# Optimization experiments

Measured on AMD Instinct MI355X. Metric: run time of the kernel, lower is better.

The kernel has to match this reference:

```python
import jax, jax.numpy as jnp
import numpy as np

NUM_HEADS = 8


def _proj(W, b, x):
    # x: [B, C, N] channel-wise 1x1 conv == matmul over channels
    return jnp.einsum('oc,bcn->bon', W, x) + b[None, :, None]


def setup_inputs() -> dict:
    key = jax.random.key(0)
    ks = jax.random.split(key, 8)
    B, C, H, W = 4, 512, 24, 24
    inp = {
        'feat0': jax.random.normal(ks[0], (B, C, H, W), jnp.float32),
        'feat1': jax.random.normal(ks[1], (B, C, H, W), jnp.float32),
        'feat2': jax.random.normal(ks[2], (B, C, H, W), jnp.float32),
        'Wq': jax.random.normal(ks[3], (C, C), jnp.float32) * 0.02,
        'bq': jnp.zeros((C,), jnp.float32),
        'Wk': jax.random.normal(ks[4], (C, C), jnp.float32) * 0.02,
        'bk': jnp.zeros((C,), jnp.float32),
        'Wv': jax.random.normal(ks[5], (C, C), jnp.float32) * 0.02,
        'bv': jnp.zeros((C,), jnp.float32),
        'Wo': jax.random.normal(ks[6], (C, C), jnp.float32) * 0.02,
        'bo': jnp.zeros((C,), jnp.float32),
    }
    return inp


def reference(feat0, feat1, feat2, Wq, bq, Wk, bk, Wv, bv, Wo, bo):
    feats = [feat0, feat1, feat2]
    B, C, H, W = feat0.shape
    h = NUM_HEADS
    d = C // h
    scale = d ** -0.5

    # Precompute K/V once per feature (the torch loop redundantly recomputes them;
    # the math is identical).
    flat = [f.reshape(B, C, H * W) for f in feats]
    K = jnp.concatenate([_proj(Wk, bk, x).reshape(B, h, d, -1) for x in flat], axis=-1)  # [B,h,d,KV]
    V = jnp.concatenate([_proj(Wv, bv, x).reshape(B, h, d, -1) for x in flat], axis=-1)  # [B,h,d,KV]

    outs = []
    for feat, x in zip(feats, flat):
        q = _proj(Wq, bq, x).reshape(B, h, d, H * W)  # [B,h,d,N]
        attn = jax.nn.softmax(jnp.einsum('bhdn,bhdm->bhnm', q, K) * scale, axis=-1)
        out = jnp.einsum('bhnm,bhdm->bhdn', attn, V).reshape(B, C, H * W)
        out = _proj(Wo, bo, out).reshape(B, C, H, W)
        outs.append(feat + out)
    return tuple(outs)
```

## Files before the change

kernel.cpp:

```cpp
#include <hip/hip_runtime.h>


using bf16x8 = __attribute__((ext_vector_type(8))) short;
using f32x4  = __attribute__((ext_vector_type(4))) float;
using f32x16 = __attribute__((ext_vector_type(16))) float;
using u32x4  = __attribute__((ext_vector_type(4))) unsigned int;
using u16x4  = __attribute__((ext_vector_type(4))) unsigned short;
using u16x8  = __attribute__((ext_vector_type(8))) unsigned short;

#define MFMA16(a, b, c) __builtin_amdgcn_mfma_f32_16x16x32_bf16((a), (b), (c), 0, 0, 0)
#define MFMA32(a, b, c) __builtin_amdgcn_mfma_f32_32x32x16_bf16((a), (b), (c), 0, 0, 0)

__device__ __forceinline__ unsigned short f2bf(float f) {
  unsigned int u = __float_as_uint(f);
  return (unsigned short)((u + 0x7fffu + ((u >> 16) & 1u)) >> 16);
}

__device__ __forceinline__ f32x16 zero16() {
  f32x16 z;
#pragma unroll
  for (int i = 0; i < 16; ++i) z[i] = 0.f;
  return z;
}

__global__ __launch_bounds__(256) void k_prep(
    const float* __restrict__ Wq, const float* __restrict__ Wk,
    const float* __restrict__ Wv, const float* __restrict__ Wo,
    const float* __restrict__ f0, const float* __restrict__ f1,
    const float* __restrict__ f2,
    unsigned short* __restrict__ Wf, unsigned short* __restrict__ Xf) {
  __shared__ unsigned short tile[64][65];
  const int bid = blockIdx.x;
  const int t = threadIdx.x;
  if (bid < 1024) {
    int idx = (bid * 256 + t) * 4;
    int p   = idx >> 18;
    int rem = idx & 262143;
    int o = rem >> 9, c0 = rem & 511;
    const float* s = p == 0 ? Wq : p == 1 ? Wk : p == 2 ? Wv : Wo;
    f32x4 v = *(const f32x4*)(s + rem);
    u16x4 pk;
    pk[0] = f2bf(v[0]); pk[1] = f2bf(v[1]); pk[2] = f2bf(v[2]); pk[3] = f2bf(v[3]);
    int mt = o >> 6, fr = (o & 63) >> 4, lr = o & 15;
    int ks = c0 >> 5, lg = (c0 & 31) >> 3, j0 = c0 & 7;
    size_t off = (size_t)((((p * 8 + mt) * 16 + ks) * 4 + fr)) * 512 +
                 (lg * 16 + lr) * 8 + j0;
    *(u16x4*)(Wf + off) = pk;
    return;
  }
  const int id = bid - 1024;
  const int nt = id % 9;
  const int ct = (id / 9) % 8;
  const int z  = id / 72;
  const int b = z / 3, f = z % 3;
  const float* src = (f == 0 ? f0 : f == 1 ? f1 : f2) + b * (512 * 576);

#pragma unroll
  for (int i = 0; i < 16; ++i) {
    int idx = i * 256 + t;
    int cc = idx >> 6, nn = idx & 63;
    tile[cc][nn] = f2bf(src[(ct * 64 + cc) * 576 + nt * 64 + nn]);
  }
  __syncthreads();
  const int ntw = f * 9 + nt;
#pragma unroll
  for (int i = 0; i < 4; ++i) {
    int slot = i * 256 + t;
    int nn = slot >> 4, cq = slot & 15;
    int cl = cq * 4;
    int c  = ct * 64 + cl;
    int fc = nn >> 4, lr = nn & 15;
    int ks = c >> 5, lg = (c & 31) >> 3, j0 = c & 7;
    u16x4 pk;
    pk[0] = tile[cl][nn]; pk[1] = tile[cl + 1][nn];
    pk[2] = tile[cl + 2][nn]; pk[3] = tile[cl + 3][nn];
    size_t off = (size_t)((((b * 27 + ntw) * 16 + ks) * 4 + fc)) * 512 +
                 (lg * 16 + lr) * 8 + j0;
    *(u16x4*)(Xf + off) = pk;
  }
}

__global__ __launch_bounds__(256) void k_gemm_qkv(
    const unsigned short* __restrict__ Wf, const unsigned short* __restrict__ Xf,
    const float* __restrict__ bq, const float* __restrict__ bk,
    const float* __restrict__ bv,
    unsigned short* __restrict__ Qf, unsigned short* __restrict__ Kf,
    unsigned short* __restrict__ Vf) {
  const int id = blockIdx.x;
  const int xcd = id & 7, s = id >> 3;
  const int b = xcd >> 1, par = xcd & 1;
  const int p = s / 54, bx = (s % 54) * 2 + par;
  const int t = threadIdx.x, w = t >> 6, l = t & 63, lg = l >> 4, lr = l & 15;
  const int wid = bx * 4 + w;
  const int mt = wid / 54, rest = wid % 54;
  const int ntw = rest >> 1, half = rest & 1;
  const unsigned short* A = Wf + (size_t)(p * 8 + mt) * 16 * 2048 + l * 8;
  const unsigned short* B = Xf + (size_t)(b * 27 + ntw) * 16 * 2048 +
                            half * 1024 + l * 8;

  f32x4 acc[4][2];
#pragma unroll
  for (int fr = 0; fr < 4; ++fr)
#pragma unroll
    for (int fc = 0; fc < 2; ++fc) acc[fr][fc] = (f32x4){0.f, 0.f, 0.f, 0.f};

#pragma unroll 2
  for (int ks = 0; ks < 16; ++ks) {
    bf16x8 af[4], bfv[2];
#pragma unroll
    for (int fr = 0; fr < 4; ++fr)
      af[fr] = *(const bf16x8*)(A + ks * 2048 + fr * 512);
#pragma unroll
    for (int fc = 0; fc < 2; ++fc)
      bfv[fc] = *(const bf16x8*)(B + ks * 2048 + fc * 512);
#pragma unroll
    for (int fr = 0; fr < 4; ++fr)
#pragma unroll
      for (int fc = 0; fc < 2; ++fc)
        acc[fr][fc] = MFMA16(af[fr], bfv[fc], acc[fr][fc]);
  }

  const float* bias = p == 0 ? bq : p == 1 ? bk : bv;
  const int bh = b * 8 + mt;
  const int ck = ntw * 2 + half;
#pragma unroll
  for (int fr = 0; fr < 4; ++fr) {
    f32x4 b4 = *(const f32x4*)(bias + mt * 64 + fr * 16 + lg * 4);
#pragma unroll
    for (int fc = 0; fc < 2; ++fc) {
      if (p < 2) {
        unsigned short* outF = (p == 0) ? Qf : Kf;
        u16x4 pk;
#pragma unroll
        for (int r = 0; r < 4; ++r) {
          float v = acc[fr][fc][r] + b4[r];
          if (p == 0) v *= 0.18033688f;
          pk[r] = f2bf(v);
        }
        size_t off = ((size_t)bh * 54 + ck) * 2048 + fr * 512 +
                     ((lg >> 1) * 32 + fc * 16 + lr) * 8 + (lg & 1) * 4;
        *(u16x4*)(outF + off) = pk;
      } else {
        size_t base = ((size_t)bh * 54 + ck) * 2048 +
                      ((fr >> 1) * 2 + fc) * 512 +
                      (((lr >> 3) & 1) * 32 + (fr & 1) * 16 + lg * 4) * 8 +
                      (lr & 7);
#pragma unroll
        for (int r = 0; r < 4; ++r)
          Vf[base + r * 8] = f2bf(acc[fr][fc][r] + b4[r]);
      }
    }
  }
}

__device__ __forceinline__ void softmax_pa(const f32x16& s, float& lsum,
                                           bf16x8& pa0, bf16x8& pa1, int hi) {
  unsigned int W[8];
  float a0 = 0.f, a1 = 0.f;
#pragma unroll
  for (int u = 0; u < 8; ++u) {
    float e0, e1;
    asm("v_exp_f32 %0, %1" : "=v"(e0) : "v"(s[2 * u]));
    asm("v_exp_f32 %0, %1" : "=v"(e1) : "v"(s[2 * u + 1]));
    a0 += e0; a1 += e1;
    asm("v_cvt_pk_bf16_f32 %0, %1, %2" : "=v"(W[u]) : "v"(e0), "v"(e1));
  }
  lsum += a0 + a1;
  unsigned int fw[2][4];
#pragma unroll
  for (int kf = 0; kf < 2; ++kf)
#pragma unroll
    for (int wd = 0; wd < 2; ++wd) {
      unsigned int lo  = W[4 * kf + wd];
      unsigned int hw  = W[4 * kf + 2 + wd];
      unsigned int pub = hi ? lo : hw;
      unsigned int rcv = (unsigned int)__shfl_xor((int)pub, 32, 64);
      fw[kf][wd]     = hi ? rcv : lo;
      fw[kf][2 + wd] = hi ? hw : rcv;
    }
  u32x4 w0, w1;
  w0[0] = fw[0][0]; w0[1] = fw[0][1]; w0[2] = fw[0][2]; w0[3] = fw[0][3];
  w1[0] = fw[1][0]; w1[1] = fw[1][1]; w1[2] = fw[1][2]; w1[3] = fw[1][3];
  pa0 = __builtin_bit_cast(bf16x8, w0);
  pa1 = __builtin_bit_cast(bf16x8, w1);
}

__global__ __launch_bounds__(128, 4) void k_attn(
    const unsigned short* __restrict__ Qf, const unsigned short* __restrict__ Kf,
    const unsigned short* __restrict__ Vf, unsigned short* __restrict__ Of) {
  const int id = blockIdx.x;
  const int xcd = id & 7, slot = id >> 3;
  const int bh = xcd * 4 + (slot / 54);
  const int qt = slot % 54;
  const int b = bh >> 3, h = bh & 7;
  const int t = threadIdx.x, w = t >> 6, l = t & 63;
  const int lr = l & 31, hi = l >> 5;

  __shared__ float Obuf[2][32][68];
  __shared__ float Lbuf[2][32];

  const unsigned short* Qb = Qf + ((size_t)bh * 54 + qt) * 2048 + l * 8;
  bf16x8 bq[4];
#pragma unroll
  for (int kf = 0; kf < 4; ++kf) bq[kf] = *(const bf16x8*)(Qb + kf * 512);

  f32x16 oacc[2];
  oacc[0] = zero16(); oacc[1] = zero16();
  float ls = 0.f;

  const unsigned short* Kb = Kf + (size_t)bh * 54 * 2048 + l * 8;
  const unsigned short* Vb = Vf + (size_t)bh * 54 * 2048 + l * 8;

#pragma unroll 1
  for (int ck = w; ck < 54; ck += 2) {
    const unsigned short* kc = Kb + ck * 2048;
    const unsigned short* vc = Vb + ck * 2048;
    bf16x8 ak[4];
#pragma unroll
    for (int i = 0; i < 4; ++i) ak[i] = *(const bf16x8*)(kc + i * 512);

    f32x16 sA = zero16();
#pragma unroll
    for (int kf = 0; kf < 4; ++kf) sA = MFMA32(ak[kf], bq[kf], sA);

    bf16x8 vb[4];
#pragma unroll
    for (int i = 0; i < 4; ++i) vb[i] = *(const bf16x8*)(vc + i * 512);

    bf16x8 pa0, pa1;
    softmax_pa(sA, ls, pa0, pa1, hi);

    oacc[0] = MFMA32(pa0, vb[0], oacc[0]);
    oacc[0] = MFMA32(pa1, vb[1], oacc[0]);
    oacc[1] = MFMA32(pa0, vb[2], oacc[1]);
    oacc[1] = MFMA32(pa1, vb[3], oacc[1]);
  }

  float lt = ls + __shfl_xor(ls, 32, 64);
  if (l < 32) Lbuf[w][lr] = lt;
#pragma unroll
  for (int dt = 0; dt < 2; ++dt)
#pragma unroll
    for (int r = 0; r < 16; ++r)
      Obuf[w][(r & 3) + 8 * (r >> 2) + 4 * hi][dt * 32 + lr] = oacc[dt][r];
  __syncthreads();

  const int n = t >> 2, dq = t & 3;
  float ltot = Lbuf[0][n] + Lbuf[1][n];
  float linv = 1.0f / ltot;
#pragma unroll
  for (int part = 0; part < 2; ++part) {
    const int d0 = dq * 16 + part * 8;
    u16x8 o8;
#pragma unroll
    for (int i = 0; i < 8; ++i) {
      float ov = Obuf[0][n][d0 + i] + Obuf[1][n][d0 + i];
      o8[i] = f2bf(ov * linv);
    }
    size_t off = (size_t)((((b * 27 + (qt >> 1)) * 16 + h * 2 + (d0 >> 5)) * 4 +
                           (qt & 1) * 2 + (n >> 4))) * 512 +
                 ((d0 >> 3) & 3) * 128 + (n & 15) * 8;
    *(u16x8*)(Of + off) = o8;
  }
}

__global__ __launch_bounds__(256) void k_gemm_out(
    const unsigned short* __restrict__ Wf, const unsigned short* __restrict__ Of,
    const float* __restrict__ bo,
    const float* __restrict__ f0, const float* __restrict__ f1,
    const float* __restrict__ f2, float* __restrict__ out) {
  const int z = blockIdx.z, b = z / 3, f = z % 3;
  const int t = threadIdx.x, w = t >> 6, l = t & 63, lg = l >> 4, lr = l & 15;
  const int wid = blockIdx.x * 4 + w;
  const int mt = wid / 18, rest = wid % 18;
  const int ntw = rest >> 1, half = rest & 1;
  const int o0 = mt * 64;
  const unsigned short* A = Wf + (size_t)(3 * 8 + mt) * 16 * 2048 + l * 8;
  const unsigned short* B = Of + (size_t)(b * 27 + f * 9 + ntw) * 16 * 2048 +
                            half * 1024 + l * 8;

  f32x4 acc[4][2];
#pragma unroll
  for (int fr = 0; fr < 4; ++fr)
#pragma unroll
    for (int fc = 0; fc < 2; ++fc) acc[fr][fc] = (f32x4){0.f, 0.f, 0.f, 0.f};

#pragma unroll 2
  for (int ks = 0; ks < 16; ++ks) {
    bf16x8 af[4], bfv[2];
#pragma unroll
    for (int fr = 0; fr < 4; ++fr)
      af[fr] = *(const bf16x8*)(A + ks * 2048 + fr * 512);
#pragma unroll
    for (int fc = 0; fc < 2; ++fc)
      bfv[fc] = *(const bf16x8*)(B + ks * 2048 + fc * 512);
#pragma unroll
    for (int fr = 0; fr < 4; ++fr)
#pragma unroll
      for (int fc = 0; fc < 2; ++fc)
        acc[fr][fc] = MFMA16(af[fr], bfv[fc], acc[fr][fc]);
  }

  const float* ft = f == 0 ? f0 : f == 1 ? f1 : f2;
#pragma unroll
  for (int fr = 0; fr < 4; ++fr) {
    f32x4 b4 = *(const f32x4*)(bo + o0 + fr * 16 + lg * 4);
#pragma unroll
    for (int fc = 0; fc < 2; ++fc) {
      int ncol = ntw * 64 + half * 32 + fc * 16 + lr;
#pragma unroll
      for (int r = 0; r < 4; ++r) {
        int o = o0 + fr * 16 + lg * 4 + r;
        out[((f * 4 + b) * 512 + o) * 576 + ncol] =
            acc[fr][fc][r] + b4[r] + ft[(b * 512 + o) * 576 + ncol];
      }
    }
  }
}

extern "C" void kernel_launch(void* const* d_in, const int* in_sizes, int n_in,
                              void* d_out, int out_size, void* d_ws, size_t ws_size,
                              hipStream_t stream) {
  const float* f0 = (const float*)d_in[0];
  const float* f1 = (const float*)d_in[1];
  const float* f2 = (const float*)d_in[2];
  const float* Wq = (const float*)d_in[3];
  const float* bq = (const float*)d_in[4];
  const float* Wk = (const float*)d_in[5];
  const float* bk = (const float*)d_in[6];
  const float* Wv = (const float*)d_in[7];
  const float* bv = (const float*)d_in[8];
  const float* Wo = (const float*)d_in[9];
  const float* bo = (const float*)d_in[10];
  float* out = (float*)d_out;

  char* ws = (char*)d_ws;
  unsigned short* Wf = (unsigned short*)(ws);
  unsigned short* Xf = (unsigned short*)(ws + 2097152);
  unsigned short* Qf = (unsigned short*)(ws + 9175040);
  unsigned short* Kf = (unsigned short*)(ws + 16252928);
  unsigned short* Vf = (unsigned short*)(ws + 23330816);
  unsigned short* Of = Xf;

  k_prep<<<dim3(1888), 256, 0, stream>>>(Wq, Wk, Wv, Wo, f0, f1, f2, Wf, Xf);
  k_gemm_qkv<<<dim3(1296), 256, 0, stream>>>(Wf, Xf, bq, bk, bv, Qf, Kf, Vf);
  k_attn<<<dim3(1728), 128, 0, stream>>>(Qf, Kf, Vf, Of);
  k_gemm_out<<<dim3(36, 1, 12), 256, 0, stream>>>(Wf, Of, bo, f0, f1, f2, out);
}
```

Baseline: 90.93 us.

## Widen GEMM warp tiles to 64x64 and permute V layout to drop softmax shuffles

Both projection GEMMs now give each wave a full 64-column tile (four B fragments) instead of 32 columns, which halves the grid and reuses each A fragment across more MFMAs. The V output layout is permuted with a bit swizzle so the attention kernel's P fragments can be fed to the PV MFMA directly. This removes the cross-lane shuffle exchange in softmax_pa. The cost is more accumulator registers per wave and fewer blocks, which may lower occupancy for the GEMMs.

```diff
diff --git a/kernel.cpp b/kernel.cpp
--- a/kernel.cpp
+++ b/kernel.cpp
@@ -89,45 +89,43 @@
   const int id = blockIdx.x;
   const int xcd = id & 7, s = id >> 3;
   const int b = xcd >> 1, par = xcd & 1;
-  const int p = s / 54, bx = (s % 54) * 2 + par;
+  const int p = s / 27, bx = (s % 27) * 2 + par;
   const int t = threadIdx.x, w = t >> 6, l = t & 63, lg = l >> 4, lr = l & 15;
   const int wid = bx * 4 + w;
-  const int mt = wid / 54, rest = wid % 54;
-  const int ntw = rest >> 1, half = rest & 1;
+  const int mt = wid / 27, ntw = wid % 27;
   const unsigned short* A = Wf + (size_t)(p * 8 + mt) * 16 * 2048 + l * 8;
-  const unsigned short* B = Xf + (size_t)(b * 27 + ntw) * 16 * 2048 +
-                            half * 1024 + l * 8;
-
-  f32x4 acc[4][2];
+  const unsigned short* B = Xf + (size_t)(b * 27 + ntw) * 16 * 2048 + l * 8;
+
+  f32x4 acc[4][4];
 #pragma unroll
   for (int fr = 0; fr < 4; ++fr)
 #pragma unroll
-    for (int fc = 0; fc < 2; ++fc) acc[fr][fc] = (f32x4){0.f, 0.f, 0.f, 0.f};
+    for (int fc = 0; fc < 4; ++fc) acc[fr][fc] = (f32x4){0.f, 0.f, 0.f, 0.f};
 
 #pragma unroll 2
   for (int ks = 0; ks < 16; ++ks) {
-    bf16x8 af[4], bfv[2];
+    bf16x8 af[4], bfv[4];
 #pragma unroll
     for (int fr = 0; fr < 4; ++fr)
       af[fr] = *(const bf16x8*)(A + ks * 2048 + fr * 512);
 #pragma unroll
-    for (int fc = 0; fc < 2; ++fc)
+    for (int fc = 0; fc < 4; ++fc)
       bfv[fc] = *(const bf16x8*)(B + ks * 2048 + fc * 512);
 #pragma unroll
     for (int fr = 0; fr < 4; ++fr)
 #pragma unroll
-      for (int fc = 0; fc < 2; ++fc)
+      for (int fc = 0; fc < 4; ++fc)
         acc[fr][fc] = MFMA16(af[fr], bfv[fc], acc[fr][fc]);
   }
 
   const float* bias = p == 0 ? bq : p == 1 ? bk : bv;
   const int bh = b * 8 + mt;
-  const int ck = ntw * 2 + half;
 #pragma unroll
   for (int fr = 0; fr < 4; ++fr) {
     f32x4 b4 = *(const f32x4*)(bias + mt * 64 + fr * 16 + lg * 4);
 #pragma unroll
-    for (int fc = 0; fc < 2; ++fc) {
+    for (int fc = 0; fc < 4; ++fc) {
+      int ck = ntw * 2 + (fc >> 1);
       if (p < 2) {
         unsigned short* outF = (p == 0) ? Qf : Kf;
         u16x4 pk;
@@ -138,13 +136,14 @@
           pk[r] = f2bf(v);
         }
         size_t off = ((size_t)bh * 54 + ck) * 2048 + fr * 512 +
-                     ((lg >> 1) * 32 + fc * 16 + lr) * 8 + (lg & 1) * 4;
+                     ((lg >> 1) * 32 + (fc & 1) * 16 + lr) * 8 + (lg & 1) * 4;
         *(u16x4*)(outF + off) = pk;
       } else {
+        int x = (lr & 3) | ((lr & 4) << 1) | ((lr & 8) >> 1);
         size_t base = ((size_t)bh * 54 + ck) * 2048 +
-                      ((fr >> 1) * 2 + fc) * 512 +
-                      (((lr >> 3) & 1) * 32 + (fr & 1) * 16 + lg * 4) * 8 +
-                      (lr & 7);
+                      ((fr >> 1) * 2 + (fc & 1)) * 512 +
+                      ((x >> 3) * 32 + (fr & 1) * 16 + lg * 4) * 8 +
+                      (x & 7);
 #pragma unroll
         for (int r = 0; r < 4; ++r)
           Vf[base + r * 8] = f2bf(acc[fr][fc][r] + b4[r]);
@@ -154,7 +153,7 @@
 }
 
 __device__ __forceinline__ void softmax_pa(const f32x16& s, float& lsum,
-                                           bf16x8& pa0, bf16x8& pa1, int hi) {
+                                           bf16x8& pa0, bf16x8& pa1) {
   unsigned int W[8];
   float a0 = 0.f, a1 = 0.f;
 #pragma unroll
@@ -166,21 +165,9 @@
     asm("v_cvt_pk_bf16_f32 %0, %1, %2" : "=v"(W[u]) : "v"(e0), "v"(e1));
   }
   lsum += a0 + a1;
-  unsigned int fw[2][4];
-#pragma unroll
-  for (int kf = 0; kf < 2; ++kf)
-#pragma unroll
-    for (int wd = 0; wd < 2; ++wd) {
-      unsigned int lo  = W[4 * kf + wd];
-      unsigned int hw  = W[4 * kf + 2 + wd];
-      unsigned int pub = hi ? lo : hw;
-      unsigned int rcv = (unsigned int)__shfl_xor((int)pub, 32, 64);
-      fw[kf][wd]     = hi ? rcv : lo;
-      fw[kf][2 + wd] = hi ? hw : rcv;
-    }
   u32x4 w0, w1;
-  w0[0] = fw[0][0]; w0[1] = fw[0][1]; w0[2] = fw[0][2]; w0[3] = fw[0][3];
-  w1[0] = fw[1][0]; w1[1] = fw[1][1]; w1[2] = fw[1][2]; w1[3] = fw[1][3];
+  w0[0] = W[0]; w0[1] = W[1]; w0[2] = W[2]; w0[3] = W[3];
+  w1[0] = W[4]; w1[1] = W[5]; w1[2] = W[6]; w1[3] = W[7];
   pa0 = __builtin_bit_cast(bf16x8, w0);
   pa1 = __builtin_bit_cast(bf16x8, w1);
 }
@@ -228,7 +215,7 @@
     for (int i = 0; i < 4; ++i) vb[i] = *(const bf16x8*)(vc + i * 512);
 
     bf16x8 pa0, pa1;
-    softmax_pa(sA, ls, pa0, pa1, hi);
+    softmax_pa(sA, ls, pa0, pa1);
 
     oacc[0] = MFMA32(pa0, vb[0], oacc[0]);
     oacc[0] = MFMA32(pa1, vb[1], oacc[0]);
@@ -272,32 +259,30 @@
   const int z = blockIdx.z, b = z / 3, f = z % 3;
   const int t = threadIdx.x, w = t >> 6, l = t & 63, lg = l >> 4, lr = l & 15;
   const int wid = blockIdx.x * 4 + w;
-  const int mt = wid / 18, rest = wid % 18;
-  const int ntw = rest >> 1, half = rest & 1;
+  const int mt = wid / 9, ntw = wid % 9;
   const int o0 = mt * 64;
   const unsigned short* A = Wf + (size_t)(3 * 8 + mt) * 16 * 2048 + l * 8;
-  const unsigned short* B = Of + (size_t)(b * 27 + f * 9 + ntw) * 16 * 2048 +
-                            half * 1024 + l * 8;
-
-  f32x4 acc[4][2];
+  const unsigned short* B = Of + (size_t)(b * 27 + f * 9 + ntw) * 16 * 2048 + l * 8;
+
+  f32x4 acc[4][4];
 #pragma unroll
   for (int fr = 0; fr < 4; ++fr)
 #pragma unroll
-    for (int fc = 0; fc < 2; ++fc) acc[fr][fc] = (f32x4){0.f, 0.f, 0.f, 0.f};
+    for (int fc = 0; fc < 4; ++fc) acc[fr][fc] = (f32x4){0.f, 0.f, 0.f, 0.f};
 
 #pragma unroll 2
   for (int ks = 0; ks < 16; ++ks) {
-    bf16x8 af[4], bfv[2];
+    bf16x8 af[4], bfv[4];
 #pragma unroll
     for (int fr = 0; fr < 4; ++fr)
       af[fr] = *(const bf16x8*)(A + ks * 2048 + fr * 512);
 #pragma unroll
-    for (int fc = 0; fc < 2; ++fc)
+    for (int fc = 0; fc < 4; ++fc)
       bfv[fc] = *(const bf16x8*)(B + ks * 2048 + fc * 512);
 #pragma unroll
     for (int fr = 0; fr < 4; ++fr)
 #pragma unroll
-      for (int fc = 0; fc < 2; ++fc)
+      for (int fc = 0; fc < 4; ++fc)
         acc[fr][fc] = MFMA16(af[fr], bfv[fc], acc[fr][fc]);
   }
 
@@ -306,8 +291,8 @@
   for (int fr = 0; fr < 4; ++fr) {
     f32x4 b4 = *(const f32x4*)(bo + o0 + fr * 16 + lg * 4);
 #pragma unroll
-    for (int fc = 0; fc < 2; ++fc) {
-      int ncol = ntw * 64 + half * 32 + fc * 16 + lr;
+    for (int fc = 0; fc < 4; ++fc) {
+      int ncol = ntw * 64 + fc * 16 + lr;
 #pragma unroll
       for (int r = 0; r < 4; ++r) {
         int o = o0 + fr * 16 + lg * 4 + r;
@@ -343,7 +328,7 @@
   unsigned short* Of = Xf;
 
   k_prep<<<dim3(1888), 256, 0, stream>>>(Wq, Wk, Wv, Wo, f0, f1, f2, Wf, Xf);
-  k_gemm_qkv<<<dim3(1296), 256, 0, stream>>>(Wf, Xf, bq, bk, bv, Qf, Kf, Vf);
+  k_gemm_qkv<<<dim3(648), 256, 0, stream>>>(Wf, Xf, bq, bk, bv, Qf, Kf, Vf);
   k_attn<<<dim3(1728), 128, 0, stream>>>(Qf, Kf, Vf, Of);
-  k_gemm_out<<<dim3(36, 1, 12), 256, 0, stream>>>(Wf, Of, bo, f0, f1, f2, out);
-}
+  k_gemm_out<<<dim3(18, 1, 12), 256, 0, stream>>>(Wf, Of, bo, f0, f1, f2, out);
+}
```

After: 96.67 us. 1.06x slower.
